# Performance work log

Hardware: AMD Instinct MI355X
Metric: run time of the kernel (lower is better)

Reference implementation:

```python
import jax, jax.numpy as jnp
import numpy as np

NEG_SLOPE = 0.01  # nn.LeakyReLU default
N_NODES = 38332
POI_LEN = 38333
CAT_LEN = 400
POI_DIM = 300
CAT_DIM = 100
GCN_CH = 64
GCN_LAYERS = 5
N_EDGES = N_NODES * 32


def leaky(x):
    return jnp.where(x >= 0, x, NEG_SLOPE * x)


def gcn_conv(x, src, dst, W, b):
    """PyG GCNConv: add self loops + symmetric normalization.
    out = D^-1/2 (A+I) D^-1/2 X W + b, deg computed with self loops."""
    n = x.shape[0]
    h = x @ W  # [N, out]
    deg = jax.ops.segment_sum(jnp.ones_like(dst, dtype=h.dtype), dst, num_segments=n) + 1.0
    dinv = jax.lax.rsqrt(deg)  # deg >= 1 always (self loop)
    norm = dinv[src] * dinv[dst]  # [E]
    agg = jax.ops.segment_sum(h[src] * norm[:, None], dst, num_segments=n)
    agg = agg + h * (1.0 / deg)[:, None]  # self-loop term: norm_ii = 1/deg_i
    return agg + b


def setup_inputs() -> dict:
    key = jax.random.key(0)
    ks = jax.random.split(key, 16)
    poi_ids = jax.random.randint(ks[0], (N_NODES, 1), 0, POI_LEN).astype(jnp.float32)
    cat_ids = jax.random.randint(ks[1], (N_NODES, 1), 0, CAT_LEN).astype(jnp.float32)
    feats = jax.random.normal(ks[2], (N_NODES, 3), dtype=jnp.float32)
    x = jnp.concatenate([poi_ids, cat_ids, feats], axis=1)  # [N,5]
    edge_index = jax.random.randint(ks[3], (2, N_EDGES), 0, N_NODES, dtype=jnp.int32)

    def glorot(k, shape):
        lim = float(np.sqrt(6.0 / (shape[0] + shape[1])))
        return jax.random.uniform(k, shape, jnp.float32, -lim, lim)

    d_in = POI_DIM + CAT_DIM + 3  # 403
    params = {
        "poi_emb": jax.random.normal(ks[4], (POI_LEN, POI_DIM), jnp.float32),
        "cat_emb": jax.random.normal(ks[5], (CAT_LEN, CAT_DIM), jnp.float32),
        "W_in": glorot(ks[6], (d_in, GCN_CH)),
        "b_in": jnp.zeros((GCN_CH,), jnp.float32),
        "gcn_Ws": jnp.stack([glorot(jax.random.fold_in(ks[7], i), (GCN_CH, GCN_CH)) for i in range(GCN_LAYERS)]),
        "gcn_bs": jnp.zeros((GCN_LAYERS, GCN_CH), jnp.float32),
        "W_out": glorot(ks[8], (GCN_CH, 1)),
        "b_out": jnp.zeros((1,), jnp.float32),
        "fc1_W": glorot(ks[9], (N_NODES, 128)),
        "fc1_b": jnp.zeros((128,), jnp.float32),
        "fc2_W": glorot(ks[10], (128, POI_LEN)),
        "fc2_b": jnpos if False else jnp.zeros((POI_LEN,), jnp.float32),
    }
    return {"x": x, "edge_index": edge_index, **params}


def reference(x, edge_index, poi_emb, cat_emb, W_in, b_in, gcn_Ws, gcn_bs, W_out, b_out, fc1_W, fc1_b, fc2_W, fc2_b):
    src, dst = edge_index[0], edge_index[1]
    poi_f = poi_emb[x[:, 0].astype(jnp.int32)]  # [N,300]
    cat_f = cat_emb[x[:, 1].astype(jnp.int32)]  # [N,100]
    feat = jnp.concatenate([poi_f, cat_f, x[:, 2:5]], axis=1)  # [N,403]
    feat = leaky(gcn_conv(feat, src, dst, W_in, b_in))
    for i in range(GCN_LAYERS):
        t = gcn_conv(feat, src, dst, gcn_Ws[i], gcn_bs[i])
        feat = leaky(t) + t  # GcnUnit: relu(temp) + temp
    feat = leaky(gcn_conv(feat, src, dst, W_out, b_out)).reshape(-1)  # [N]
    h = jax.nn.relu(feat @ fc1_W + fc1_b)
    out = jax.nn.relu(h @ fc2_W + fc2_b)  # [poi_len]
    return out
```

## Files before the change

### kernel.cpp

```cpp
#include <hip/hip_runtime.h>
#include <hip/hip_bf16.h>

#define N_NODES 38332
#define POI_LEN 38333
#define CAT_LEN 400
#define POI_DIM 300
#define CAT_DIM 100
#define N_EDGES (N_NODES * 32)
#define NEG_SLOPE 0.01f
#define NSLOT 96
#define B1 ((N_NODES + 127) / 128)
#define SPLIT_CHUNK 2048
#define NSPLIT ((N_EDGES + SPLIT_CHUNK - 1) / SPLIT_CHUNK)
#define BCAP 8192

typedef __attribute__((ext_vector_type(8))) short short8;
typedef __attribute__((ext_vector_type(4))) float f32x4;

__device__ __forceinline__ unsigned short f2bf(float f) {
  unsigned u = __float_as_uint(f);
  u += 0x7fff + ((u >> 16) & 1);
  return (unsigned short)(u >> 16);
}
__device__ __forceinline__ float bflo(unsigned u) {
  return __uint_as_float(u << 16);
}
__device__ __forceinline__ float bfhi(unsigned u) {
  return __uint_as_float(u & 0xffff0000u);
}
__device__ __forceinline__ void acc8(float4& a0, float4& a1, uint4 v) {
  a0.x += bflo(v.x); a0.y += bfhi(v.x); a0.z += bflo(v.y); a0.w += bfhi(v.y);
  a1.x += bflo(v.z); a1.y += bfhi(v.z); a1.z += bflo(v.w); a1.w += bfhi(v.w);
}


#define WFIN_ELEMS (13 * 2048)
#define WFGCN_ELEMS (5 * 4096)

__global__ __launch_bounds__(256) void k_prep(const float* __restrict__ W_in,
                                              const float* __restrict__ gcn_Ws,
                                              unsigned short* __restrict__ wf_in,
                                              unsigned short* __restrict__ wf_gcn,
                                              int* __restrict__ bcnt,
                                              float* __restrict__ h128) {
  int idx = blockIdx.x * 256 + threadIdx.x;
  if (idx < B1) bcnt[idx] = 0;
  if (idx < 128) h128[idx] = 0.f;
  if (idx < WFIN_ELEMS) {
    int j = idx & 7, n = (idx >> 3) & 63, q = (idx >> 9) & 3, ks = idx >> 11;
    int k = ks * 32 + q * 8 + j;
    wf_in[idx] = f2bf((k < 400) ? W_in[k * 64 + n] : 0.f);
  } else if (idx < WFIN_ELEMS + WFGCN_ELEMS) {
    int t = idx - WFIN_ELEMS;
    int l = t >> 12, i = t & 4095;
    int j = i & 7, n = (i >> 3) & 63, q = (i >> 9) & 3, ks = i >> 11;
    int k = ks * 32 + q * 8 + j;
    wf_gcn[t] = f2bf(gcn_Ws[(size_t)l * 4096 + k * 64 + n]);
  }
}


__global__ __launch_bounds__(256) void k_split(const int* __restrict__ src,
                                               const int* __restrict__ dst,
                                               int* __restrict__ bcnt,
                                               int* __restrict__ staging) {
  __shared__ int hist[B1];
  __shared__ int lbase[B1];
  __shared__ int lcur[B1];
  int tid = threadIdx.x;
  int base = blockIdx.x * SPLIT_CHUNK;
  int n = N_EDGES - base;
  if (n > SPLIT_CHUNK) n = SPLIT_CHUNK;
  for (int b = tid; b < B1; b += 256) {
    hist[b] = 0;
    lcur[b] = 0;
  }
  __syncthreads();
  for (int i = tid; i < n; i += 256) atomicAdd(&hist[dst[base + i] >> 7], 1);
  __syncthreads();
  for (int b = tid; b < B1; b += 256) {
    int c = hist[b];
    lbase[b] = c ? atomicAdd(&bcnt[b], c) : 0;
  }
  __syncthreads();
  for (int i = tid; i < n; i += 256) {
    int d = dst[base + i];
    int s = src[base + i];
    int b = d >> 7;
    int off = atomicAdd(&lcur[b], 1);
    staging[(size_t)b * BCAP + lbase[b] + off] = (s << 7) | (d & 127);
  }
}

__global__ __launch_bounds__(256) void k_place(const int* __restrict__ staging,
                                               const int* __restrict__ bcnt,
                                               int* __restrict__ csr,
                                               int* __restrict__ cnt,
                                               float* __restrict__ dinv) {
  __shared__ int cur[128];
  int b = blockIdx.x;
  int tid = threadIdx.x;
  int d0 = b * 128;
  int nd = N_NODES - d0;
  if (nd > 128) nd = 128;
  int cnt_b = bcnt[b];
  const int* st = staging + (size_t)b * BCAP;
  if (tid < 128) cur[tid] = 0;
  __syncthreads();
  for (int i = tid; i < cnt_b; i += 256) {
    int pk = st[i];
    int dl = pk & 127;
    int pos = atomicAdd(&cur[dl], 1);
    csr[(size_t)(d0 + dl) * NSLOT + pos] = pk >> 7;
  }
  __syncthreads();
  if (tid < nd) {
    int v = cur[tid];
    cnt[d0 + tid] = v;
    dinv[d0 + tid] = 1.0f / sqrtf((float)(v + 1));
  }
}


__global__ __launch_bounds__(256) void k_front(
    const float* __restrict__ x, const float* __restrict__ poi_emb,
    const float* __restrict__ cat_emb, const float* __restrict__ W_in,
    const unsigned short* __restrict__ wf_in, const float* __restrict__ dinv,
    unsigned short* __restrict__ hs) {
  constexpr int RS = 424;
  __shared__ unsigned short sA[16 * RS];
  __shared__ float sC[16 * 68];
  __shared__ int sPid[16], sCid[16];
  __shared__ float sX[16][3];
  __shared__ float sDinv[16];
  int tid = threadIdx.x;
  int row0 = blockIdx.x * 16;
  if (tid < 16) {
    int row = row0 + tid;
    if (row < N_NODES) {
      sPid[tid] = (int)x[row * 5 + 0];
      sCid[tid] = (int)x[row * 5 + 1];
      sX[tid][0] = x[row * 5 + 2];
      sX[tid][1] = x[row * 5 + 3];
      sX[tid][2] = x[row * 5 + 4];
      sDinv[tid] = dinv[row];
    } else {
      sPid[tid] = 0; sCid[tid] = 0;
      sX[tid][0] = sX[tid][1] = sX[tid][2] = 0.f;
      sDinv[tid] = 0.f;
    }
  }
  __syncthreads();
  for (int idx = tid; idx < 16 * 104; idx += 256) {
    int r = idx / 104;
    int k = (idx - r * 104) * 4;
    ushort4 o = {0, 0, 0, 0};
    if (k < 400 && row0 + r < N_NODES) {
      float4 f;
      if (k < 300) f = *(const float4*)(poi_emb + (size_t)sPid[r] * 300 + k);
      else         f = *(const float4*)(cat_emb + (size_t)sCid[r] * 100 + (k - 300));
      o.x = f2bf(f.x); o.y = f2bf(f.y); o.z = f2bf(f.z); o.w = f2bf(f.w);
    }
    *(ushort4*)&sA[r * RS + k] = o;
  }
  __syncthreads();
  int lane = tid & 63, wv = tid >> 6;
  int c = lane & 15, q = lane >> 4, n0 = wv * 16;
  f32x4 acc = {0.f, 0.f, 0.f, 0.f};
  const unsigned short* arow = &sA[c * RS];
#pragma unroll
  for (int ks = 0; ks < 13; ks++) {
    short8 af = *(const short8*)(arow + ks * 32 + q * 8);
    short8 bf = *(const short8*)(wf_in + ((size_t)((ks * 4 + q) * 64 + n0 + c)) * 8);
    acc = __builtin_amdgcn_mfma_f32_16x16x32_bf16(af, bf, acc, 0, 0, 0);
  }
#pragma unroll
  for (int r = 0; r < 4; r++) sC[(q * 4 + r) * 68 + n0 + c] = acc[r];
  __syncthreads();
  for (int idx = tid; idx < 16 * 64; idx += 256) {
    int r = idx >> 6, col = idx & 63;
    int row = row0 + r;
    if (row < N_NODES) {
      float v = sC[r * 68 + col] + sX[r][0] * W_in[400 * 64 + col] +
                sX[r][1] * W_in[401 * 64 + col] + sX[r][2] * W_in[402 * 64 + col];
      hs[(size_t)row * 64 + col] = f2bf(v * sDinv[r]);
    }
  }
}


template <int MODE>
__global__ __launch_bounds__(256) void k_agg(const unsigned short* __restrict__ hs,
                                             const int* __restrict__ cnt,
                                             const int* __restrict__ csr,
                                             const float* __restrict__ dinv,
                                             const float* __restrict__ bias,
                                             const unsigned short* __restrict__ Wf,
                                             unsigned short* __restrict__ hs_next,
                                             const float* __restrict__ W_out,
                                             float* __restrict__ hs1) {
  __shared__ unsigned short sA[16 * 72];
  __shared__ float sC[4 * 68];
  int tid = threadIdx.x;
  int lane = tid & 63;
  int wv = tid >> 6;
  int node = blockIdx.x * 4 + wv;
  int eslot = lane >> 3;
  int ch8 = lane & 7;
  if (MODE != 2) {
    for (int i = tid; i < 216; i += 256)
      *(ushort4*)&sA[288 + i * 4] = (ushort4){0, 0, 0, 0};
  }
  int deg = cnt[node];
  float dn = dinv[node];
  const int* crow = csr + (size_t)node * NSLOT;
  uint4 sv = {0, 0, 0, 0};
  if (lane < 8) sv = *(const uint4*)(hs + (size_t)node * 64 + ch8 * 8);
  float4 a0 = {0.f, 0.f, 0.f, 0.f}, a1 = a0;
  for (int j = eslot * 4; j < deg; j += 32) {
    int4 s4 = *(const int4*)(crow + j);
    if (j + 4 <= deg) {
      uint4 v0 = *(const uint4*)(hs + (size_t)s4.x * 64 + ch8 * 8);
      uint4 v1 = *(const uint4*)(hs + (size_t)s4.y * 64 + ch8 * 8);
      uint4 v2 = *(const uint4*)(hs + (size_t)s4.z * 64 + ch8 * 8);
      uint4 v3 = *(const uint4*)(hs + (size_t)s4.w * 64 + ch8 * 8);
      acc8(a0, a1, v0); acc8(a0, a1, v1); acc8(a0, a1, v2); acc8(a0, a1, v3);
    } else {
      if (j + 1 <= deg) {
        uint4 v = *(const uint4*)(hs + (size_t)s4.x * 64 + ch8 * 8);
        acc8(a0, a1, v);
      }
      if (j + 2 <= deg) {
        uint4 v = *(const uint4*)(hs + (size_t)s4.y * 64 + ch8 * 8);
        acc8(a0, a1, v);
      }
      if (j + 3 <= deg) {
        uint4 v = *(const uint4*)(hs + (size_t)s4.z * 64 + ch8 * 8);
        acc8(a0, a1, v);
      }
    }
  }
#pragma unroll
  for (int off = 8; off <= 32; off <<= 1) {
    a0.x += __shfl_xor(a0.x, off, 64);
    a0.y += __shfl_xor(a0.y, off, 64);
    a0.z += __shfl_xor(a0.z, off, 64);
    a0.w += __shfl_xor(a0.w, off, 64);
    a1.x += __shfl_xor(a1.x, off, 64);
    a1.y += __shfl_xor(a1.y, off, 64);
    a1.z += __shfl_xor(a1.z, off, 64);
    a1.w += __shfl_xor(a1.w, off, 64);
  }
  if (lane < 8) {
    float4 bb0 = *(const float4*)(bias + ch8 * 8);
    float4 bb1 = *(const float4*)(bias + ch8 * 8 + 4);
    float4 t0, t1;
    t0.x = dn * (a0.x + bflo(sv.x)) + bb0.x;
    t0.y = dn * (a0.y + bfhi(sv.x)) + bb0.y;
    t0.z = dn * (a0.z + bflo(sv.y)) + bb0.z;
    t0.w = dn * (a0.w + bfhi(sv.y)) + bb0.w;
    t1.x = dn * (a1.x + bflo(sv.z)) + bb1.x;
    t1.y = dn * (a1.y + bfhi(sv.z)) + bb1.y;
    t1.z = dn * (a1.z + bflo(sv.w)) + bb1.z;
    t1.w = dn * (a1.w + bfhi(sv.w)) + bb1.w;
    float4 l0, l1, o0, o1;
    l0.x = (t0.x >= 0.f) ? t0.x : NEG_SLOPE * t0.x;
    l0.y = (t0.y >= 0.f) ? t0.y : NEG_SLOPE * t0.y;
    l0.z = (t0.z >= 0.f) ? t0.z : NEG_SLOPE * t0.z;
    l0.w = (t0.w >= 0.f) ? t0.w : NEG_SLOPE * t0.w;
    l1.x = (t1.x >= 0.f) ? t1.x : NEG_SLOPE * t1.x;
    l1.y = (t1.y >= 0.f) ? t1.y : NEG_SLOPE * t1.y;
    l1.z = (t1.z >= 0.f) ? t1.z : NEG_SLOPE * t1.z;
    l1.w = (t1.w >= 0.f) ? t1.w : NEG_SLOPE * t1.w;
    if (MODE == 0) {
      o0 = l0; o1 = l1;
    } else {
      o0.x = l0.x + t0.x; o0.y = l0.y + t0.y; o0.z = l0.z + t0.z; o0.w = l0.w + t0.w;
      o1.x = l1.x + t1.x; o1.y = l1.y + t1.y; o1.z = l1.z + t1.z; o1.w = l1.w + t1.w;
    }
    if (MODE == 2) {
      float4 w0 = *(const float4*)(W_out + ch8 * 8);
      float4 w1 = *(const float4*)(W_out + ch8 * 8 + 4);
      float p = o0.x * w0.x + o0.y * w0.y + o0.z * w0.z + o0.w * w0.w +
                o1.x * w1.x + o1.y * w1.y + o1.z * w1.z + o1.w * w1.w;
      p += __shfl_xor(p, 1, 64);
      p += __shfl_xor(p, 2, 64);
      p += __shfl_xor(p, 4, 64);
      if (lane == 0) hs1[node] = p * dn;
    } else {
      uint4 pk;
      pk.x = (unsigned)f2bf(o0.x) | ((unsigned)f2bf(o0.y) << 16);
      pk.y = (unsigned)f2bf(o0.z) | ((unsigned)f2bf(o0.w) << 16);
      pk.z = (unsigned)f2bf(o1.x) | ((unsigned)f2bf(o1.y) << 16);
      pk.w = (unsigned)f2bf(o1.z) | ((unsigned)f2bf(o1.w) << 16);
      *(uint4*)&sA[wv * 72 + ch8 * 8] = pk;
    }
  }
  if (MODE != 2) {
    __syncthreads();
    int c = lane & 15, q = lane >> 4, n0 = wv * 16;
    f32x4 acc = {0.f, 0.f, 0.f, 0.f};
    const unsigned short* arow = &sA[c * 72];
#pragma unroll
    for (int ks = 0; ks < 2; ks++) {
      short8 af = *(const short8*)(arow + ks * 32 + q * 8);
      short8 bf = *(const short8*)(Wf + ((size_t)((ks * 4 + q) * 64 + n0 + c)) * 8);
      acc = __builtin_amdgcn_mfma_f32_16x16x32_bf16(af, bf, acc, 0, 0, 0);
    }
    if (q == 0) {
#pragma unroll
      for (int r = 0; r < 4; r++) sC[r * 68 + n0 + c] = acc[r];
    }
    __syncthreads();
    if (tid < 128) {
      int r = tid >> 5, c2 = (tid & 31) * 2;
      int row = blockIdx.x * 4 + r;
      float dr = dinv[row];
      unsigned lo = f2bf(sC[r * 68 + c2] * dr);
      unsigned hi = f2bf(sC[r * 68 + c2 + 1] * dr);
      *(unsigned*)(hs_next + (size_t)row * 64 + c2) = lo | (hi << 16);
    }
  }
}


__global__ __launch_bounds__(256) void k_out_agg(const float* __restrict__ hs1,
                                                 const int* __restrict__ cnt,
                                                 const int* __restrict__ csr,
                                                 const float* __restrict__ dinv,
                                                 const float* __restrict__ b_out,
                                                 float* __restrict__ g) {
  int lane = threadIdx.x & 63;
  int w = threadIdx.x >> 6;
  int node = blockIdx.x * 4 + w;
  int deg = cnt[node];
  const int* crow = csr + (size_t)node * NSLOT;
  float acc = 0.f;
  for (int e = lane; e < deg; e += 64) acc += hs1[crow[e]];
#pragma unroll
  for (int off = 32; off; off >>= 1) acc += __shfl_xor(acc, off, 64);
  if (lane == 0) {
    float t = dinv[node] * (acc + hs1[node]) + b_out[0];
    g[node] = (t >= 0.f) ? t : NEG_SLOPE * t;
  }
}


__global__ __launch_bounds__(128) void k_fc1(const float* __restrict__ g,
                                             const float* __restrict__ fc1_W,
                                             float* __restrict__ h128) {
  int j = threadIdx.x;
  int base = blockIdx.x * 32;
  int end = base + 32;
  if (end > N_NODES) end = N_NODES;
  float acc = 0.f;
  int i = base;
  for (; i + 4 <= end; i += 4) {
    acc += g[i + 0] * fc1_W[(size_t)(i + 0) * 128 + j];
    acc += g[i + 1] * fc1_W[(size_t)(i + 1) * 128 + j];
    acc += g[i + 2] * fc1_W[(size_t)(i + 2) * 128 + j];
    acc += g[i + 3] * fc1_W[(size_t)(i + 3) * 128 + j];
  }
  for (; i < end; i++) acc += g[i] * fc1_W[(size_t)i * 128 + j];
  atomicAdd(&h128[j], acc);
}

__global__ __launch_bounds__(256) void k_fc2(const float* __restrict__ h128raw,
                                             const float* __restrict__ fc1_b,
                                             const float* __restrict__ fc2_W,
                                             const float* __restrict__ fc2_b,
                                             float* __restrict__ out) {
  __shared__ float sh[128];
  int tid = threadIdx.x;
  if (tid < 128) {
    float v = h128raw[tid] + fc1_b[tid];
    sh[tid] = (v > 0.f) ? v : 0.f;
  }
  __syncthreads();
  int p = blockIdx.x * 256 + tid;
  if (p < POI_LEN) {
    float acc = fc2_b[p];
#pragma unroll 8
    for (int j = 0; j < 128; j++) acc += sh[j] * fc2_W[(size_t)j * POI_LEN + p];
    out[p] = (acc > 0.f) ? acc : 0.f;
  }
}


extern "C" void kernel_launch(void* const* d_in, const int* in_sizes, int n_in,
                              void* d_out, int out_size, void* d_ws, size_t ws_size,
                              hipStream_t stream) {
  const float* x       = (const float*)d_in[0];
  const int*   ei      = (const int*)d_in[1];
  const float* poi_emb = (const float*)d_in[2];
  const float* cat_emb = (const float*)d_in[3];
  const float* W_in    = (const float*)d_in[4];
  const float* b_in    = (const float*)d_in[5];
  const float* gcn_Ws  = (const float*)d_in[6];
  const float* gcn_bs  = (const float*)d_in[7];
  const float* W_out   = (const float*)d_in[8];
  const float* b_out   = (const float*)d_in[9];
  const float* fc1_W   = (const float*)d_in[10];
  const float* fc1_b   = (const float*)d_in[11];
  const float* fc2_W   = (const float*)d_in[12];
  const float* fc2_b   = (const float*)d_in[13];
  const int* src = ei;
  const int* dst = ei + N_EDGES;

  char* p = (char*)d_ws;
  auto take = [&](size_t bytes) {
    char* r = p;
    p += (bytes + 255) & ~(size_t)255;
    return r;
  };
  int*   cnt  = (int*)take((size_t)N_NODES * 4);
  float* dinv = (float*)take((size_t)N_NODES * 4);
  int*   bcnt = (int*)take((size_t)B1 * 4);
  int*   csr  = (int*)take((size_t)N_NODES * NSLOT * 4);
  unsigned short* hsA = (unsigned short*)take((size_t)N_NODES * 64 * 2);
  unsigned short* hsB = (unsigned short*)take((size_t)N_NODES * 64 * 2);
  float* hs1  = (float*)take((size_t)N_NODES * 4);
  float* g    = (float*)take((size_t)N_NODES * 4);
  float* h128 = (float*)take(128 * 4);
  unsigned short* wf_in  = (unsigned short*)take((size_t)WFIN_ELEMS * 2);
  unsigned short* wf_gcn = (unsigned short*)take((size_t)WFGCN_ELEMS * 2);
  int* staging = (int*)hsA;
  float* out = (float*)d_out;

  const int nb4 = N_NODES / 4;
  const int nb16 = (N_NODES + 15) / 16;

  k_prep<<<(WFIN_ELEMS + WFGCN_ELEMS + 255) / 256, 256, 0, stream>>>(
      W_in, gcn_Ws, wf_in, wf_gcn, bcnt, h128);
  k_split<<<NSPLIT, 256, 0, stream>>>(src, dst, bcnt, staging);
  k_place<<<B1, 256, 0, stream>>>(staging, bcnt, csr, cnt, dinv);

  k_front<<<nb16, 256, 0, stream>>>(x, poi_emb, cat_emb, W_in, wf_in, dinv, hsA);

  k_agg<0><<<nb4, 256, 0, stream>>>(hsA, cnt, csr, dinv, b_in,
                                    wf_gcn + 0 * 4096, hsB, nullptr, nullptr);
  k_agg<1><<<nb4, 256, 0, stream>>>(hsB, cnt, csr, dinv, gcn_bs + 0 * 64,
                                    wf_gcn + 1 * 4096, hsA, nullptr, nullptr);
  k_agg<1><<<nb4, 256, 0, stream>>>(hsA, cnt, csr, dinv, gcn_bs + 1 * 64,
                                    wf_gcn + 2 * 4096, hsB, nullptr, nullptr);
  k_agg<1><<<nb4, 256, 0, stream>>>(hsB, cnt, csr, dinv, gcn_bs + 2 * 64,
                                    wf_gcn + 3 * 4096, hsA, nullptr, nullptr);
  k_agg<1><<<nb4, 256, 0, stream>>>(hsA, cnt, csr, dinv, gcn_bs + 3 * 64,
                                    wf_gcn + 4 * 4096, hsB, nullptr, nullptr);
  k_agg<2><<<nb4, 256, 0, stream>>>(hsB, cnt, csr, dinv, gcn_bs + 4 * 64,
                                    nullptr, nullptr, W_out, hs1);

  k_out_agg<<<nb4, 256, 0, stream>>>(hs1, cnt, csr, dinv, b_out, g);
  k_fc1<<<(N_NODES + 31) / 32, 128, 0, stream>>>(g, fc1_W, h128);
  k_fc2<<<(POI_LEN + 255) / 256, 256, 0, stream>>>(h128, fc1_b, fc2_W, fc2_b, out);
}
```

Before: 414.6 us.

## Use 16-bit CSR indices, pack dinv and degree, parallelize edge placement

```diff
diff --git a/kernel.cpp b/kernel.cpp
--- a/kernel.cpp
+++ b/kernel.cpp
@@ -42,9 +42,11 @@
                                               unsigned short* __restrict__ wf_in,
                                               unsigned short* __restrict__ wf_gcn,
                                               int* __restrict__ bcnt,
+                                              int* __restrict__ cnt,
                                               float* __restrict__ h128) {
   int idx = blockIdx.x * 256 + threadIdx.x;
   if (idx < B1) bcnt[idx] = 0;
+  if (idx < N_NODES) cnt[idx] = 0;
   if (idx < 128) h128[idx] = 0.f;
   if (idx < WFIN_ELEMS) {
     int j = idx & 7, n = (idx >> 3) & 63, q = (idx >> 9) & 3, ks = idx >> 11;
@@ -94,30 +96,21 @@
 
 __global__ __launch_bounds__(256) void k_place(const int* __restrict__ staging,
                                                const int* __restrict__ bcnt,
-                                               int* __restrict__ csr,
                                                int* __restrict__ cnt,
-                                               float* __restrict__ dinv) {
-  __shared__ int cur[128];
-  int b = blockIdx.x;
-  int tid = threadIdx.x;
+                                               unsigned short* __restrict__ csr) {
+  int b = blockIdx.x >> 2, c = blockIdx.x & 3;
+  int n = bcnt[b];
+  int per = (n + 3) >> 2;
+  int i0 = c * per;
+  int i1 = i0 + per;
+  if (i1 > n) i1 = n;
+  const int* st = staging + (size_t)b * BCAP;
   int d0 = b * 128;
-  int nd = N_NODES - d0;
-  if (nd > 128) nd = 128;
-  int cnt_b = bcnt[b];
-  const int* st = staging + (size_t)b * BCAP;
-  if (tid < 128) cur[tid] = 0;
-  __syncthreads();
-  for (int i = tid; i < cnt_b; i += 256) {
+  for (int i = i0 + threadIdx.x; i < i1; i += 256) {
     int pk = st[i];
-    int dl = pk & 127;
-    int pos = atomicAdd(&cur[dl], 1);
-    csr[(size_t)(d0 + dl) * NSLOT + pos] = pk >> 7;
-  }
-  __syncthreads();
-  if (tid < nd) {
-    int v = cur[tid];
-    cnt[d0 + tid] = v;
-    dinv[d0 + tid] = 1.0f / sqrtf((float)(v + 1));
+    int d = d0 + (pk & 127);
+    int pos = atomicAdd(&cnt[d], 1);
+    csr[(size_t)d * NSLOT + pos] = (unsigned short)(pk >> 7);
   }
 }
 
@@ -125,8 +118,8 @@
 __global__ __launch_bounds__(256) void k_front(
     const float* __restrict__ x, const float* __restrict__ poi_emb,
     const float* __restrict__ cat_emb, const float* __restrict__ W_in,
-    const unsigned short* __restrict__ wf_in, const float* __restrict__ dinv,
-    unsigned short* __restrict__ hs) {
+    const unsigned short* __restrict__ wf_in, const int* __restrict__ cnt,
+    float2* __restrict__ nd, unsigned short* __restrict__ hs) {
   constexpr int RS = 424;
   __shared__ unsigned short sA[16 * RS];
   __shared__ float sC[16 * 68];
@@ -143,7 +136,10 @@
       sX[tid][0] = x[row * 5 + 2];
       sX[tid][1] = x[row * 5 + 3];
       sX[tid][2] = x[row * 5 + 4];
-      sDinv[tid] = dinv[row];
+      int deg = cnt[row];
+      float dn = 1.0f / sqrtf((float)(deg + 1));
+      sDinv[tid] = dn;
+      nd[row] = make_float2(dn, (float)deg);
     } else {
       sPid[tid] = 0; sCid[tid] = 0;
       sX[tid][0] = sX[tid][1] = sX[tid][2] = 0.f;
@@ -191,9 +187,8 @@
 
 template <int MODE>
 __global__ __launch_bounds__(256) void k_agg(const unsigned short* __restrict__ hs,
-                                             const int* __restrict__ cnt,
-                                             const int* __restrict__ csr,
-                                             const float* __restrict__ dinv,
+                                             const float2* __restrict__ nd,
+                                             const unsigned short* __restrict__ csr,
                                              const float* __restrict__ bias,
                                              const unsigned short* __restrict__ Wf,
                                              unsigned short* __restrict__ hs_next,
@@ -201,6 +196,7 @@
                                              float* __restrict__ hs1) {
   __shared__ unsigned short sA[16 * 72];
   __shared__ float sC[4 * 68];
+  __shared__ float sDn[4];
   int tid = threadIdx.x;
   int lane = tid & 63;
   int wv = tid >> 6;
@@ -211,14 +207,16 @@
     for (int i = tid; i < 216; i += 256)
       *(ushort4*)&sA[288 + i * 4] = (ushort4){0, 0, 0, 0};
   }
-  int deg = cnt[node];
-  float dn = dinv[node];
-  const int* crow = csr + (size_t)node * NSLOT;
+  float2 meta = nd[node];
+  float dn = meta.x;
+  int deg = (int)meta.y;
+  const unsigned short* crow = csr + (size_t)node * NSLOT;
   uint4 sv = {0, 0, 0, 0};
   if (lane < 8) sv = *(const uint4*)(hs + (size_t)node * 64 + ch8 * 8);
+  if (MODE != 2 && lane == 8) sDn[wv] = dn;
   float4 a0 = {0.f, 0.f, 0.f, 0.f}, a1 = a0;
   for (int j = eslot * 4; j < deg; j += 32) {
-    int4 s4 = *(const int4*)(crow + j);
+    ushort4 s4 = *(const ushort4*)(crow + j);
     if (j + 4 <= deg) {
       uint4 v0 = *(const uint4*)(hs + (size_t)s4.x * 64 + ch8 * 8);
       uint4 v1 = *(const uint4*)(hs + (size_t)s4.y * 64 + ch8 * 8);
@@ -315,7 +313,7 @@
     if (tid < 128) {
       int r = tid >> 5, c2 = (tid & 31) * 2;
       int row = blockIdx.x * 4 + r;
-      float dr = dinv[row];
+      float dr = sDn[r];
       unsigned lo = f2bf(sC[r * 68 + c2] * dr);
       unsigned hi = f2bf(sC[r * 68 + c2 + 1] * dr);
       *(unsigned*)(hs_next + (size_t)row * 64 + c2) = lo | (hi << 16);
@@ -325,22 +323,22 @@
 
 
 __global__ __launch_bounds__(256) void k_out_agg(const float* __restrict__ hs1,
-                                                 const int* __restrict__ cnt,
-                                                 const int* __restrict__ csr,
-                                                 const float* __restrict__ dinv,
+                                                 const float2* __restrict__ nd,
+                                                 const unsigned short* __restrict__ csr,
                                                  const float* __restrict__ b_out,
                                                  float* __restrict__ g) {
   int lane = threadIdx.x & 63;
   int w = threadIdx.x >> 6;
   int node = blockIdx.x * 4 + w;
-  int deg = cnt[node];
-  const int* crow = csr + (size_t)node * NSLOT;
+  float2 meta = nd[node];
+  int deg = (int)meta.y;
+  const unsigned short* crow = csr + (size_t)node * NSLOT;
   float acc = 0.f;
   for (int e = lane; e < deg; e += 64) acc += hs1[crow[e]];
 #pragma unroll
   for (int off = 32; off; off >>= 1) acc += __shfl_xor(acc, off, 64);
   if (lane == 0) {
-    float t = dinv[node] * (acc + hs1[node]) + b_out[0];
+    float t = meta.x * (acc + hs1[node]) + b_out[0];
     g[node] = (t >= 0.f) ? t : NEG_SLOPE * t;
   }
 }
@@ -413,10 +411,10 @@
     p += (bytes + 255) & ~(size_t)255;
     return r;
   };
-  int*   cnt  = (int*)take((size_t)N_NODES * 4);
-  float* dinv = (float*)take((size_t)N_NODES * 4);
-  int*   bcnt = (int*)take((size_t)B1 * 4);
-  int*   csr  = (int*)take((size_t)N_NODES * NSLOT * 4);
+  int*    cnt  = (int*)take((size_t)N_NODES * 4);
+  float2* nd   = (float2*)take((size_t)N_NODES * 8);
+  int*    bcnt = (int*)take((size_t)B1 * 4);
+  unsigned short* csr = (unsigned short*)take((size_t)N_NODES * NSLOT * 2);
   unsigned short* hsA = (unsigned short*)take((size_t)N_NODES * 64 * 2);
   unsigned short* hsB = (unsigned short*)take((size_t)N_NODES * 64 * 2);
   float* hs1  = (float*)take((size_t)N_NODES * 4);
@@ -431,26 +429,27 @@
   const int nb16 = (N_NODES + 15) / 16;
 
   k_prep<<<(WFIN_ELEMS + WFGCN_ELEMS + 255) / 256, 256, 0, stream>>>(
-      W_in, gcn_Ws, wf_in, wf_gcn, bcnt, h128);
+      W_in, gcn_Ws, wf_in, wf_gcn, bcnt, cnt, h128);
   k_split<<<NSPLIT, 256, 0, stream>>>(src, dst, bcnt, staging);
-  k_place<<<B1, 256, 0, stream>>>(staging, bcnt, csr, cnt, dinv);
-
-  k_front<<<nb16, 256, 0, stream>>>(x, poi_emb, cat_emb, W_in, wf_in, dinv, hsA);
-
-  k_agg<0><<<nb4, 256, 0, stream>>>(hsA, cnt, csr, dinv, b_in,
-                                    wf_gcn + 0 * 4096, hsB, nullptr, nullptr);
-  k_agg<1><<<nb4, 256, 0, stream>>>(hsB, cnt, csr, dinv, gcn_bs + 0 * 64,
+  k_place<<<B1 * 4, 256, 0, stream>>>(staging, bcnt, cnt, csr);
+
+  k_front<<<nb16, 256, 0, stream>>>(x, poi_emb, cat_emb, W_in, wf_in, cnt, nd,
+                                    hsA);
+
+  k_agg<0><<<nb4, 256, 0, stream>>>(hsA, nd, csr, b_in, wf_gcn + 0 * 4096, hsB,
+                                    nullptr, nullptr);
+  k_agg<1><<<nb4, 256, 0, stream>>>(hsB, nd, csr, gcn_bs + 0 * 64,
                                     wf_gcn + 1 * 4096, hsA, nullptr, nullptr);
-  k_agg<1><<<nb4, 256, 0, stream>>>(hsA, cnt, csr, dinv, gcn_bs + 1 * 64,
+  k_agg<1><<<nb4, 256, 0, stream>>>(hsA, nd, csr, gcn_bs + 1 * 64,
                                     wf_gcn + 2 * 4096, hsB, nullptr, nullptr);
-  k_agg<1><<<nb4, 256, 0, stream>>>(hsB, cnt, csr, dinv, gcn_bs + 2 * 64,
+  k_agg<1><<<nb4, 256, 0, stream>>>(hsB, nd, csr, gcn_bs + 2 * 64,
                                     wf_gcn + 3 * 4096, hsA, nullptr, nullptr);
-  k_agg<1><<<nb4, 256, 0, stream>>>(hsA, cnt, csr, dinv, gcn_bs + 3 * 64,
+  k_agg<1><<<nb4, 256, 0, stream>>>(hsA, nd, csr, gcn_bs + 3 * 64,
                                     wf_gcn + 4 * 4096, hsB, nullptr, nullptr);
-  k_agg<2><<<nb4, 256, 0, stream>>>(hsB, cnt, csr, dinv, gcn_bs + 4 * 64,
-                                    nullptr, nullptr, W_out, hs1);
-
-  k_out_agg<<<nb4, 256, 0, stream>>>(hs1, cnt, csr, dinv, b_out, g);
+  k_agg<2><<<nb4, 256, 0, stream>>>(hsB, nd, csr, gcn_bs + 4 * 64, nullptr,
+                                    nullptr, W_out, hs1);
+
+  k_out_agg<<<nb4, 256, 0, stream>>>(hs1, nd, csr, b_out, g);
   k_fc1<<<(N_NODES + 31) / 32, 128, 0, stream>>>(g, fc1_W, h128);
   k_fc2<<<(POI_LEN + 255) / 256, 256, 0, stream>>>(h128, fc1_b, fc2_W, fc2_b, out);
 }
```

After: 431.3 us. 4.0% more time.
